# Kernel optimization log

Measured on AMD Instinct MI355X. Metric: run time of the kernel, lower is better.

## Reference

```python
import jax, jax.numpy as jnp
import numpy as np

ALPHA = 2.0
EROSIONS = 10
# 2D cross structuring element * 0.2, same as cv.getStructuringElement(cv.MORPH_CROSS,(3,3))*0.2
KERNEL2D = jnp.array([[0.0, 0.2, 0.0],
                      [0.2, 0.2, 0.2],
                      [0.0, 0.2, 0.0]], dtype=jnp.float32)


def setup_inputs() -> dict:
    key = jax.random.key(0)
    k1, k2 = jax.random.split(key)
    B, C, H, W = 8, 8, 512, 512
    x = jax.random.uniform(k1, (B, C, H, W), dtype=jnp.float32)
    y = jax.random.uniform(k2, (B, C, H, W), dtype=jnp.float32)
    return {"x": x, "y": y}


def reference(x, y):
    # bound = (pred - target)^2, shape (B, C, H, W)
    bound = (x - y) ** 2
    B, C, H, W = bound.shape
    # batch all (b, cls) images into one conv: (B*C, 1, H, W)
    cur = bound.reshape(B * C, 1, H, W)
    kern = KERNEL2D.reshape(1, 1, 3, 3)  # OIHW; kernel is symmetric so conv == correlate

    def step(carry, k):
        cur, acc = carry
        # scipy convolve(mode='constant', cval=0) == SAME zero-padded conv
        dil = jax.lax.conv_general_dilated(cur, kern, window_strides=(1, 1),
                                           padding='SAME',
                                           dimension_numbers=('NCHW', 'OIHW', 'NCHW'))
        ero = jnp.maximum(dil - 0.5, 0.0)
        # per-image global min-max normalization iff ptp != 0
        mn = ero.min(axis=(1, 2, 3), keepdims=True)
        mx = ero.max(axis=(1, 2, 3), keepdims=True)
        ptp = mx - mn
        normed = (ero - mn) / jnp.where(ptp > 0, ptp, 1.0)
        ero = jnp.where(ptp > 0, normed, ero)
        acc = acc + ero * (k.astype(ero.dtype) + 1.0) ** ALPHA
        return (ero, acc), None

    (_, eroted), _ = jax.lax.scan(step, (cur, jnp.zeros_like(cur)),
                                  jnp.arange(EROSIONS))
    # batch_dice=False -> plain mean over everything
    return eroted.mean()
```

## Files before the change

kernel.cpp:

```cpp
#include <hip/hip_runtime.h>

#define IMGS 64
#define HH 512
#define WW 512
#define NPIX (HH * WW)
#define STEPS 10
#define RSTRIP 16
#define BLKS_PER_IMG 32
#define NBLK (IMGS * BLKS_PER_IMG)
#define WPI 64

template <int FIRST, int STORE>
__global__ __launch_bounds__(128) void kconv(const float* __restrict__ xg,
                                             const float* __restrict__ yg,
                                             const float* __restrict__ src,
                                             float* __restrict__ dst,
                                             const float2* __restrict__ prevMM,
                                             float2* __restrict__ pmm,
                                             double* __restrict__ psum) {
    const int bid = blockIdx.x;
    const int swz = (bid & 7) * (NBLK / 8) + (bid >> 3);
    const int img = swz >> 5;
    const int blk = swz & 31;
    const int tid = threadIdx.x;
    const int w = tid >> 6;
    const int lane = tid & 63;
    const int vc = w * 64 + lane;
    const int ys = blk * RSTRIP;
    const size_t base = (size_t)img * NPIX;

    float scale = 1.0f, off = 0.0f;
    if (!FIRST) {
        float2 a = prevMM[img * WPI + lane];
        float tmn = a.x, tmx = a.y;
        #pragma unroll
        for (int o2 = 32; o2 > 0; o2 >>= 1) {
            tmn = fminf(tmn, __shfl_xor(tmn, o2));
            tmx = fmaxf(tmx, __shfl_xor(tmx, o2));
        }
        float ptp = tmx - tmn;
        if (ptp > 0.0f) { scale = 1.0f / ptp; off = tmn * scale; }
    }

    const float4* xv = (const float4*)(xg + base);
    const float4* yv = (const float4*)(yg + base);
    const float4* sv = (const float4*)(src + base);

    auto ld4 = [&](int r) -> float4 {
        if (FIRST) {
            float4 a = xv[r * 128 + vc];
            float4 b = yv[r * 128 + vc];
            float4 v;
            v.x = (a.x - b.x) * (a.x - b.x);
            v.y = (a.y - b.y) * (a.y - b.y);
            v.z = (a.z - b.z) * (a.z - b.z);
            v.w = (a.w - b.w) * (a.w - b.w);
            return v;
        } else {
            float4 v = sv[r * 128 + vc];
            v.x = fmaf(v.x, scale, -off);
            v.y = fmaf(v.y, scale, -off);
            v.z = fmaf(v.z, scale, -off);
            v.w = fmaf(v.w, scale, -off);
            return v;
        }
    };
    auto ld1 = [&](int r, int pcol) -> float {
        if (FIRST) {
            float d = xg[base + r * WW + pcol] - yg[base + r * WW + pcol];
            return d * d;
        } else {
            return fmaf(src[base + r * WW + pcol], scale, -off);
        }
    };

    const float4 z4 = make_float4(0.f, 0.f, 0.f, 0.f);
    float4 pm1 = (ys > 0) ? ld4(ys - 1) : z4;
    float4 p0 = ld4(ys);

    float tmin = __uint_as_float(0x7f800000u);
    float tmax = 0.0f;
    float tsum = 0.0f;
    float4* dv = (float4*)(dst + base);

    #pragma unroll
    for (int i = 0; i < RSTRIP; ++i) {
        const int y = ys + i;
        float4 p1 = (y + 1 < HH) ? ld4(y + 1) : z4;

        float lf = __shfl_up(p0.w, 1);
        float rt = __shfl_down(p0.x, 1);
        if (lane == 0)  lf = (vc > 0)   ? ld1(y, vc * 4 - 1) : 0.0f;
        if (lane == 63) rt = (vc < 127) ? ld1(y, vc * 4 + 4) : 0.0f;

        float4 e;
        e.x = 0.2f * (pm1.x + p1.x + lf   + p0.x + p0.y);
        e.y = 0.2f * (pm1.y + p1.y + p0.x + p0.y + p0.z);
        e.z = 0.2f * (pm1.z + p1.z + p0.y + p0.z + p0.w);
        e.w = 0.2f * (pm1.w + p1.w + p0.z + p0.w + rt);
        e.x = fmaxf(e.x - 0.5f, 0.0f);
        e.y = fmaxf(e.y - 0.5f, 0.0f);
        e.z = fmaxf(e.z - 0.5f, 0.0f);
        e.w = fmaxf(e.w - 0.5f, 0.0f);

        if (STORE) dv[y * 128 + vc] = e;

        tmin = fminf(tmin, fminf(fminf(e.x, e.y), fminf(e.z, e.w)));
        tmax = fmaxf(tmax, fmaxf(fmaxf(e.x, e.y), fmaxf(e.z, e.w)));
        tsum += (e.x + e.y) + (e.z + e.w);

        pm1 = p0;
        p0 = p1;
    }

    double dsum = (double)tsum;
    #pragma unroll
    for (int o2 = 32; o2 > 0; o2 >>= 1) {
        tmin = fminf(tmin, __shfl_down(tmin, o2));
        tmax = fmaxf(tmax, __shfl_down(tmax, o2));
        dsum += __shfl_down(dsum, o2);
    }

    if (lane == 0) {
        const int idx = img * WPI + blk * 2 + w;
        pmm[idx] = make_float2(tmin, tmax);
        psum[idx] = dsum;
    }
}

__global__ __launch_bounds__(64) void kfin1(const float2* __restrict__ pmm,
                                            const double* __restrict__ psum,
                                            double* __restrict__ perImg) {
    const int img = blockIdx.x;
    const int lane = threadIdx.x;
    double tot = 0.0;
    for (int k = 0; k < STEPS; ++k) {
        const int o = (k * IMGS + img) * WPI;
        float2 a = pmm[o + lane];
        double s = psum[o + lane];
        float tmn = a.x;
        float tmx = a.y;
        #pragma unroll
        for (int o2 = 32; o2 > 0; o2 >>= 1) {
            tmn = fminf(tmn, __shfl_xor(tmn, o2));
            tmx = fmaxf(tmx, __shfl_xor(tmx, o2));
            s += __shfl_xor(s, o2);
        }
        float ptp = tmx - tmn;
        double sn = (ptp > 0.0f)
                        ? (s - (double)NPIX * (double)tmn) / (double)ptp
                        : s;
        tot += sn * (double)((k + 1) * (k + 1));
    }
    if (lane == 0) perImg[img] = tot;
}

__global__ void kfin2(const double* __restrict__ perImg,
                      float* __restrict__ out) {
    double v = perImg[threadIdx.x];
    #pragma unroll
    for (int o2 = 32; o2 > 0; o2 >>= 1) v += __shfl_down(v, o2);
    if (threadIdx.x == 0)
        out[0] = (float)(v / ((double)IMGS * (double)NPIX));
}

extern "C" void kernel_launch(void* const* d_in, const int* in_sizes, int n_in,
                              void* d_out, int out_size, void* d_ws, size_t ws_size,
                              hipStream_t stream) {
    const float* x = (const float*)d_in[0];
    const float* y = (const float*)d_in[1];
    float* out = (float*)d_out;

    char* ws = (char*)d_ws;
    const size_t bufBytes = (size_t)IMGS * NPIX * sizeof(float);
    float* bufA = (float*)ws;
    float* bufB = (float*)(ws + bufBytes);
    char* p = ws + 2 * bufBytes;
    float2* pmm = (float2*)p;        p += (size_t)STEPS * IMGS * WPI * sizeof(float2);
    double* psum = (double*)p;       p += (size_t)STEPS * IMGS * WPI * sizeof(double);
    double* perImg = (double*)p;

    kconv<1, 1><<<NBLK, 128, 0, stream>>>(x, y, nullptr, bufA, nullptr,
                                          pmm, psum);
    float* cur = bufA;
    float* nxt = bufB;
    for (int k = 1; k < STEPS - 1; ++k) {
        kconv<0, 1><<<NBLK, 128, 0, stream>>>(
            nullptr, nullptr, cur, nxt,
            pmm + (size_t)(k - 1) * IMGS * WPI,
            pmm + (size_t)k * IMGS * WPI,
            psum + (size_t)k * IMGS * WPI);
        float* tmp = cur; cur = nxt; nxt = tmp;
    }
    kconv<0, 0><<<NBLK, 128, 0, stream>>>(
        nullptr, nullptr, cur, nullptr,
        pmm + (size_t)(STEPS - 2) * IMGS * WPI,
        pmm + (size_t)(STEPS - 1) * IMGS * WPI,
        psum + (size_t)(STEPS - 1) * IMGS * WPI);

    kfin1<<<IMGS, 64, 0, stream>>>(pmm, psum, perImg);
    kfin2<<<1, 64, 0, stream>>>(perImg, out);
}
```

Before: 218.6 us.

## Fuse pairs of erosion steps to skip storing intermediate buffers

```diff
diff --git a/kernel.cpp b/kernel.cpp
--- a/kernel.cpp
+++ b/kernel.cpp
@@ -128,6 +128,175 @@
     }
 }
 
+__global__ __launch_bounds__(128) void kfuse(const float* __restrict__ src,
+                                             float* __restrict__ dst,
+                                             const float2* __restrict__ mmA,
+                                             const float2* __restrict__ mmB,
+                                             float2* __restrict__ pmm,
+                                             double* __restrict__ psum) {
+    const int bid = blockIdx.x;
+    const int swz = (bid & 7) * (NBLK / 8) + (bid >> 3);
+    const int img = swz >> 5;
+    const int blk = swz & 31;
+    const int tid = threadIdx.x;
+    const int w = tid >> 6;
+    const int lane = tid & 63;
+    const int vc = w * 64 + lane;
+    const int ys = blk * RSTRIP;
+    const size_t base = (size_t)img * NPIX;
+
+    float2 a1 = mmA[img * WPI + lane];
+    float2 a2 = mmB[img * WPI + lane];
+    float mn1 = a1.x, mx1 = a1.y, mn2 = a2.x, mx2 = a2.y;
+    #pragma unroll
+    for (int o2 = 32; o2 > 0; o2 >>= 1) {
+        mn1 = fminf(mn1, __shfl_xor(mn1, o2));
+        mx1 = fmaxf(mx1, __shfl_xor(mx1, o2));
+        mn2 = fminf(mn2, __shfl_xor(mn2, o2));
+        mx2 = fmaxf(mx2, __shfl_xor(mx2, o2));
+    }
+    float s1 = 1.0f, o1 = 0.0f;
+    { float p = mx1 - mn1; if (p > 0.0f) { s1 = 1.0f / p; o1 = mn1 * s1; } }
+    float s2 = 1.0f, o2v = 0.0f;
+    { float p = mx2 - mn2; if (p > 0.0f) { s2 = 1.0f / p; o2v = mn2 * s2; } }
+
+    const float4* sv = (const float4*)(src + base);
+    auto ld4 = [&](int r) -> float4 {
+        float4 v = sv[r * 128 + vc];
+        v.x = fmaf(v.x, s1, -o1);
+        v.y = fmaf(v.y, s1, -o1);
+        v.z = fmaf(v.z, s1, -o1);
+        v.w = fmaf(v.w, s1, -o1);
+        return v;
+    };
+    auto nat = [&](int r, int c) -> float {
+        if (r < 0 || r >= HH || c < 0 || c >= WW) return 0.0f;
+        return fmaf(src[base + r * WW + c], s1, -o1);
+    };
+
+    struct ERow { float4 m; float mL, mR; };
+    auto eroRow = [&](const float4& r0, const float4& r1, const float4& r2,
+                      int yy) -> ERow {
+        float lf = __shfl_up(r1.w, 1);
+        float rt = __shfl_down(r1.x, 1);
+        if (lane == 0)  lf = nat(yy, vc * 4 - 1);
+        if (lane == 63) rt = nat(yy, vc * 4 + 4);
+        float4 e;
+        e.x = 0.2f * (r0.x + r2.x + lf   + r1.x + r1.y);
+        e.y = 0.2f * (r0.y + r2.y + r1.x + r1.y + r1.z);
+        e.z = 0.2f * (r0.z + r2.z + r1.y + r1.z + r1.w);
+        e.w = 0.2f * (r0.w + r2.w + r1.z + r1.w + rt);
+        e.x = fmaxf(e.x - 0.5f, 0.0f);
+        e.y = fmaxf(e.y - 0.5f, 0.0f);
+        e.z = fmaxf(e.z - 0.5f, 0.0f);
+        e.w = fmaxf(e.w - 0.5f, 0.0f);
+        ERow o;
+        o.m.x = fmaf(e.x, s2, -o2v);
+        o.m.y = fmaf(e.y, s2, -o2v);
+        o.m.z = fmaf(e.z, s2, -o2v);
+        o.m.w = fmaf(e.w, s2, -o2v);
+        o.mL = 0.0f; o.mR = 0.0f;
+        if (lane == 0) {
+            const int pL = vc * 4 - 1;
+            if (pL >= 0) {
+                float eL = 0.2f * (nat(yy - 1, pL) + nat(yy + 1, pL) +
+                                   nat(yy, pL - 1) + nat(yy, pL) +
+                                   nat(yy, pL + 1));
+                eL = fmaxf(eL - 0.5f, 0.0f);
+                o.mL = fmaf(eL, s2, -o2v);
+            }
+        }
+        if (lane == 63) {
+            const int pR = vc * 4 + 4;
+            if (pR < WW) {
+                float eR = 0.2f * (nat(yy - 1, pR) + nat(yy + 1, pR) +
+                                   nat(yy, pR - 1) + nat(yy, pR) +
+                                   nat(yy, pR + 1));
+                eR = fmaxf(eR - 0.5f, 0.0f);
+                o.mR = fmaf(eR, s2, -o2v);
+            }
+        }
+        return o;
+    };
+
+    const float4 z4 = make_float4(0.f, 0.f, 0.f, 0.f);
+    ERow zer; zer.m = z4; zer.mL = 0.0f; zer.mR = 0.0f;
+
+    ERow em1, e0;
+    float4 fa, fb;
+    if (ys == 0) {
+        em1 = zer;
+        float4 f0 = ld4(0);
+        float4 f1 = ld4(1);
+        e0 = eroRow(z4, f0, f1, 0);
+        fa = f0; fb = f1;
+    } else {
+        float4 fm2 = (ys >= 2) ? ld4(ys - 2) : z4;
+        float4 fm1 = ld4(ys - 1);
+        float4 f0 = ld4(ys);
+        em1 = eroRow(fm2, fm1, f0, ys - 1);
+        float4 f1 = ld4(ys + 1);
+        e0 = eroRow(fm1, f0, f1, ys);
+        fa = f0; fb = f1;
+    }
+
+    float tmin = __uint_as_float(0x7f800000u);
+    float tmax = 0.0f;
+    float tsum = 0.0f;
+    float4* dv = (float4*)(dst + base);
+
+    #pragma unroll
+    for (int i = 0; i < RSTRIP; ++i) {
+        const int y = ys + i;
+        ERow ep1;
+        if (y + 1 < HH) {
+            float4 fc = (y + 2 < HH) ? ld4(y + 2) : z4;
+            ep1 = eroRow(fa, fb, fc, y + 1);
+            fa = fb; fb = fc;
+        } else {
+            ep1 = zer;
+        }
+
+        float lf = __shfl_up(e0.m.w, 1);
+        float rt = __shfl_down(e0.m.x, 1);
+        if (lane == 0)  lf = e0.mL;
+        if (lane == 63) rt = e0.mR;
+
+        float4 g;
+        g.x = 0.2f * (em1.m.x + ep1.m.x + lf     + e0.m.x + e0.m.y);
+        g.y = 0.2f * (em1.m.y + ep1.m.y + e0.m.x + e0.m.y + e0.m.z);
+        g.z = 0.2f * (em1.m.z + ep1.m.z + e0.m.y + e0.m.z + e0.m.w);
+        g.w = 0.2f * (em1.m.w + ep1.m.w + e0.m.z + e0.m.w + rt);
+        g.x = fmaxf(g.x - 0.5f, 0.0f);
+        g.y = fmaxf(g.y - 0.5f, 0.0f);
+        g.z = fmaxf(g.z - 0.5f, 0.0f);
+        g.w = fmaxf(g.w - 0.5f, 0.0f);
+
+        dv[y * 128 + vc] = g;
+
+        tmin = fminf(tmin, fminf(fminf(g.x, g.y), fminf(g.z, g.w)));
+        tmax = fmaxf(tmax, fmaxf(fmaxf(g.x, g.y), fmaxf(g.z, g.w)));
+        tsum += (g.x + g.y) + (g.z + g.w);
+
+        em1 = e0;
+        e0 = ep1;
+    }
+
+    double dsum = (double)tsum;
+    #pragma unroll
+    for (int o2 = 32; o2 > 0; o2 >>= 1) {
+        tmin = fminf(tmin, __shfl_down(tmin, o2));
+        tmax = fmaxf(tmax, __shfl_down(tmax, o2));
+        dsum += __shfl_down(dsum, o2);
+    }
+
+    if (lane == 0) {
+        const int idx = img * WPI + blk * 2 + w;
+        pmm[idx] = make_float2(tmin, tmax);
+        psum[idx] = dsum;
+    }
+}
+
 __global__ __launch_bounds__(64) void kfin1(const float2* __restrict__ pmm,
                                             const double* __restrict__ psum,
                                             double* __restrict__ perImg) {
@@ -180,23 +349,32 @@
     double* psum = (double*)p;       p += (size_t)STEPS * IMGS * WPI * sizeof(double);
     double* perImg = (double*)p;
 
+    const size_t SLOT = (size_t)IMGS * WPI;
+
     kconv<1, 1><<<NBLK, 128, 0, stream>>>(x, y, nullptr, bufA, nullptr,
                                           pmm, psum);
     float* cur = bufA;
     float* nxt = bufB;
-    for (int k = 1; k < STEPS - 1; ++k) {
-        kconv<0, 1><<<NBLK, 128, 0, stream>>>(
-            nullptr, nullptr, cur, nxt,
-            pmm + (size_t)(k - 1) * IMGS * WPI,
-            pmm + (size_t)k * IMGS * WPI,
-            psum + (size_t)k * IMGS * WPI);
+    for (int pr = 0; pr < 4; ++pr) {
+        const int k = 2 * pr + 1;
+        kconv<0, 0><<<NBLK, 128, 0, stream>>>(
+            nullptr, nullptr, cur, nullptr,
+            pmm + (size_t)(k - 1) * SLOT,
+            pmm + (size_t)k * SLOT,
+            psum + (size_t)k * SLOT);
+        kfuse<<<NBLK, 128, 0, stream>>>(
+            cur, nxt,
+            pmm + (size_t)(k - 1) * SLOT,
+            pmm + (size_t)k * SLOT,
+            pmm + (size_t)(k + 1) * SLOT,
+            psum + (size_t)(k + 1) * SLOT);
         float* tmp = cur; cur = nxt; nxt = tmp;
     }
     kconv<0, 0><<<NBLK, 128, 0, stream>>>(
         nullptr, nullptr, cur, nullptr,
-        pmm + (size_t)(STEPS - 2) * IMGS * WPI,
-        pmm + (size_t)(STEPS - 1) * IMGS * WPI,
-        psum + (size_t)(STEPS - 1) * IMGS * WPI);
+        pmm + (size_t)8 * SLOT,
+        pmm + (size_t)9 * SLOT,
+        psum + (size_t)9 * SLOT);
 
     kfin1<<<IMGS, 64, 0, stream>>>(pmm, psum, perImg);
     kfin2<<<1, 64, 0, stream>>>(perImg, out);
```

Result: slower. 260.4 us (+19.1%).

## Fuse erosion steps pairwise with stats-only pass and LDS halo recompute

Applied to the files above, without the earlier changes.

```diff
diff --git a/kernel.cpp b/kernel.cpp
--- a/kernel.cpp
+++ b/kernel.cpp
@@ -6,8 +6,9 @@
 #define NPIX (HH * WW)
 #define STEPS 10
 #define RSTRIP 16
-#define BLKS_PER_IMG 32
-#define NBLK (IMGS * BLKS_PER_IMG)
+#define NBLK (IMGS * 32)
+#define FROWS 8
+#define NBLKF (IMGS * 64)
 #define WPI 64
 
 template <int FIRST, int STORE>
@@ -128,6 +129,173 @@
     }
 }
 
+template <int FIRST, int STORE>
+__global__ __launch_bounds__(128) void kfuse(const float* __restrict__ xg,
+                                             const float* __restrict__ yg,
+                                             const float* __restrict__ src,
+                                             float* __restrict__ dst,
+                                             const float2* __restrict__ mmA,
+                                             const float2* __restrict__ mmB,
+                                             float2* __restrict__ pmm,
+                                             double* __restrict__ psum) {
+    const int bid = blockIdx.x;
+    const int swz = (bid & 7) * (NBLKF / 8) + (bid >> 3);
+    const int img = swz >> 6;
+    const int blk = swz & 63;
+    const int tid = threadIdx.x;
+    const int w = tid >> 6;
+    const int lane = tid & 63;
+    const int vc = w * 64 + lane;
+    const int ys = blk * FROWS;
+    const size_t base = (size_t)img * NPIX;
+
+    __shared__ float lds[10][512];
+
+    float s1 = 1.0f, o1 = 0.0f;
+    if (!FIRST) {
+        float2 a = mmA[img * WPI + lane];
+        float mn = a.x, mx = a.y;
+        #pragma unroll
+        for (int o2 = 32; o2 > 0; o2 >>= 1) {
+            mn = fminf(mn, __shfl_xor(mn, o2));
+            mx = fmaxf(mx, __shfl_xor(mx, o2));
+        }
+        float p = mx - mn;
+        if (p > 0.0f) { s1 = 1.0f / p; o1 = mn * s1; }
+    }
+    float s2 = 1.0f, o2v = 0.0f;
+    {
+        float2 a = mmB[img * WPI + lane];
+        float mn = a.x, mx = a.y;
+        #pragma unroll
+        for (int o2 = 32; o2 > 0; o2 >>= 1) {
+            mn = fminf(mn, __shfl_xor(mn, o2));
+            mx = fmaxf(mx, __shfl_xor(mx, o2));
+        }
+        float p = mx - mn;
+        if (p > 0.0f) { s2 = 1.0f / p; o2v = mn * s2; }
+    }
+
+    const float4* xv = (const float4*)(xg + base);
+    const float4* yv = (const float4*)(yg + base);
+    const float4* sv = (const float4*)(src + base);
+
+    auto ld4 = [&](int r) -> float4 {
+        if (FIRST) {
+            float4 a = xv[r * 128 + vc];
+            float4 b = yv[r * 128 + vc];
+            float4 v;
+            v.x = (a.x - b.x) * (a.x - b.x);
+            v.y = (a.y - b.y) * (a.y - b.y);
+            v.z = (a.z - b.z) * (a.z - b.z);
+            v.w = (a.w - b.w) * (a.w - b.w);
+            return v;
+        } else {
+            float4 v = sv[r * 128 + vc];
+            v.x = fmaf(v.x, s1, -o1);
+            v.y = fmaf(v.y, s1, -o1);
+            v.z = fmaf(v.z, s1, -o1);
+            v.w = fmaf(v.w, s1, -o1);
+            return v;
+        }
+    };
+    auto ld1 = [&](int r, int pcol) -> float {
+        if (FIRST) {
+            float d = xg[base + r * WW + pcol] - yg[base + r * WW + pcol];
+            return d * d;
+        } else {
+            return fmaf(src[base + r * WW + pcol], s1, -o1);
+        }
+    };
+
+    const float4 z4 = make_float4(0.f, 0.f, 0.f, 0.f);
+
+    float4 fm1 = (ys >= 2) ? ld4(ys - 2) : z4;
+    float4 f0  = (ys >= 1) ? ld4(ys - 1) : z4;
+    #pragma unroll
+    for (int j = 0; j < FROWS + 2; ++j) {
+        const int r = ys - 1 + j;
+        float4 f1 = (r + 1 < HH) ? ld4(r + 1) : z4;
+        float4 e = z4;
+        if (r >= 0 && r < HH) {
+            float lf = __shfl_up(f0.w, 1);
+            float rt = __shfl_down(f0.x, 1);
+            if (lane == 0)  lf = (vc > 0)   ? ld1(r, vc * 4 - 1) : 0.0f;
+            if (lane == 63) rt = (vc < 127) ? ld1(r, vc * 4 + 4) : 0.0f;
+            float4 t;
+            t.x = 0.2f * (fm1.x + f1.x + lf   + f0.x + f0.y);
+            t.y = 0.2f * (fm1.y + f1.y + f0.x + f0.y + f0.z);
+            t.z = 0.2f * (fm1.z + f1.z + f0.y + f0.z + f0.w);
+            t.w = 0.2f * (fm1.w + f1.w + f0.z + f0.w + rt);
+            t.x = fmaxf(t.x - 0.5f, 0.0f);
+            t.y = fmaxf(t.y - 0.5f, 0.0f);
+            t.z = fmaxf(t.z - 0.5f, 0.0f);
+            t.w = fmaxf(t.w - 0.5f, 0.0f);
+            e.x = fmaf(t.x, s2, -o2v);
+            e.y = fmaf(t.y, s2, -o2v);
+            e.z = fmaf(t.z, s2, -o2v);
+            e.w = fmaf(t.w, s2, -o2v);
+        }
+        *(float4*)&lds[j][4 * vc] = e;
+        fm1 = f0;
+        f0 = f1;
+    }
+    __syncthreads();
+
+    float tmin = __uint_as_float(0x7f800000u);
+    float tmax = 0.0f;
+    float tsum = 0.0f;
+    float4* dv = (float4*)(dst + base);
+
+    #pragma unroll
+    for (int i = 0; i < FROWS; ++i) {
+        const int y = ys + i;
+        float4 up = *(const float4*)&lds[i][4 * vc];
+        float4 c4 = *(const float4*)&lds[i + 1][4 * vc];
+        float4 dn = *(const float4*)&lds[i + 2][4 * vc];
+        float lf = (vc > 0)   ? lds[i + 1][4 * vc - 1] : 0.0f;
+        float rt = (vc < 127) ? lds[i + 1][4 * vc + 4] : 0.0f;
+
+        float4 g;
+        g.x = 0.2f * (up.x + dn.x + lf   + c4.x + c4.y);
+        g.y = 0.2f * (up.y + dn.y + c4.x + c4.y + c4.z);
+        g.z = 0.2f * (up.z + dn.z + c4.y + c4.z + c4.w);
+        g.w = 0.2f * (up.w + dn.w + c4.z + c4.w + rt);
+        g.x = fmaxf(g.x - 0.5f, 0.0f);
+        g.y = fmaxf(g.y - 0.5f, 0.0f);
+        g.z = fmaxf(g.z - 0.5f, 0.0f);
+        g.w = fmaxf(g.w - 0.5f, 0.0f);
+
+        if (STORE) dv[y * 128 + vc] = g;
+
+        tmin = fminf(tmin, fminf(fminf(g.x, g.y), fminf(g.z, g.w)));
+        tmax = fmaxf(tmax, fmaxf(fmaxf(g.x, g.y), fmaxf(g.z, g.w)));
+        tsum += (g.x + g.y) + (g.z + g.w);
+    }
+
+    double dsum = (double)tsum;
+    #pragma unroll
+    for (int o2 = 32; o2 > 0; o2 >>= 1) {
+        tmin = fminf(tmin, __shfl_down(tmin, o2));
+        tmax = fmaxf(tmax, __shfl_down(tmax, o2));
+        dsum += __shfl_down(dsum, o2);
+    }
+
+    __syncthreads();
+    if (lane == 0) {
+        lds[0][w] = tmin;
+        lds[0][2 + w] = tmax;
+        ((double*)&lds[2][0])[w] = dsum;
+    }
+    __syncthreads();
+    if (tid == 0) {
+        const int idx = img * WPI + blk;
+        pmm[idx] = make_float2(fminf(lds[0][0], lds[0][1]),
+                               fmaxf(lds[0][2], lds[0][3]));
+        psum[idx] = ((double*)&lds[2][0])[0] + ((double*)&lds[2][0])[1];
+    }
+}
+
 __global__ __launch_bounds__(64) void kfin1(const float2* __restrict__ pmm,
                                             const double* __restrict__ psum,
                                             double* __restrict__ perImg) {
@@ -180,23 +348,41 @@
     double* psum = (double*)p;       p += (size_t)STEPS * IMGS * WPI * sizeof(double);
     double* perImg = (double*)p;
 
-    kconv<1, 1><<<NBLK, 128, 0, stream>>>(x, y, nullptr, bufA, nullptr,
+    const size_t SLOT = (size_t)IMGS * WPI;
+
+    kconv<1, 0><<<NBLK, 128, 0, stream>>>(x, y, nullptr, nullptr, nullptr,
                                           pmm, psum);
+    kfuse<1, 1><<<NBLKF, 128, 0, stream>>>(x, y, nullptr, bufA,
+                                           nullptr, pmm,
+                                           pmm + SLOT, psum + SLOT);
     float* cur = bufA;
     float* nxt = bufB;
-    for (int k = 1; k < STEPS - 1; ++k) {
-        kconv<0, 1><<<NBLK, 128, 0, stream>>>(
+    for (int pr = 1; pr <= 3; ++pr) {
+        const int k = 2 * pr;
+        kconv<0, 0><<<NBLK, 128, 0, stream>>>(
+            nullptr, nullptr, cur, nullptr,
+            pmm + (size_t)(k - 1) * SLOT,
+            pmm + (size_t)k * SLOT,
+            psum + (size_t)k * SLOT);
+        kfuse<0, 1><<<NBLKF, 128, 0, stream>>>(
             nullptr, nullptr, cur, nxt,
-            pmm + (size_t)(k - 1) * IMGS * WPI,
-            pmm + (size_t)k * IMGS * WPI,
-            psum + (size_t)k * IMGS * WPI);
+            pmm + (size_t)(k - 1) * SLOT,
+            pmm + (size_t)k * SLOT,
+            pmm + (size_t)(k + 1) * SLOT,
+            psum + (size_t)(k + 1) * SLOT);
         float* tmp = cur; cur = nxt; nxt = tmp;
     }
     kconv<0, 0><<<NBLK, 128, 0, stream>>>(
         nullptr, nullptr, cur, nullptr,
-        pmm + (size_t)(STEPS - 2) * IMGS * WPI,
-        pmm + (size_t)(STEPS - 1) * IMGS * WPI,
-        psum + (size_t)(STEPS - 1) * IMGS * WPI);
+        pmm + (size_t)7 * SLOT,
+        pmm + (size_t)8 * SLOT,
+        psum + (size_t)8 * SLOT);
+    kfuse<0, 0><<<NBLKF, 128, 0, stream>>>(
+        nullptr, nullptr, cur, nullptr,
+        pmm + (size_t)7 * SLOT,
+        pmm + (size_t)8 * SLOT,
+        pmm + (size_t)9 * SLOT,
+        psum + (size_t)9 * SLOT);
 
     kfin1<<<IMGS, 64, 0, stream>>>(pmm, psum, perImg);
     kfin2<<<1, 64, 0, stream>>>(perImg, out);
```

Measured after the change: 269.9 us. +23.4%, slower.
